# Optimization experiments

Measured on AMD Instinct MI355X. Metric: run time of the kernel, lower is better.

The kernel has to match this reference:

```python
import jax, jax.numpy as jnp
import numpy as np

N_NODES = 100000
N_EDGES = 1600000
NFEAT, NHID, NCLASS = 128, 64, 16


def setup_inputs() -> dict:
    key = jax.random.key(0)
    ks = jax.random.split(key, 6)
    x = jax.random.normal(ks[0], (N_NODES, NFEAT), dtype=jnp.float32)
    src = jax.random.randint(ks[1], (N_EDGES,), 0, N_NODES)
    dst = jax.random.randint(ks[2], (N_EDGES,), 0, N_NODES)
    # Glorot-ish init for the two GraphConv weights, zero bias (DGL default)
    W1 = jax.random.normal(ks[3], (NFEAT, NHID), dtype=jnp.float32) * (1.0 / np.sqrt(NFEAT))
    b1 = jnp.zeros((NHID,), dtype=jnp.float32)
    W2 = jax.random.normal(ks[4], (NHID, NCLASS), dtype=jnp.float32) * (1.0 / np.sqrt(NHID))
    b2 = jnp.zeros((NCLASS,), dtype=jnp.float32)
    return {"x": x, "src": src, "dst": dst, "W1": W1, "b1": b1, "W2": W2, "b2": b2}


def _graph_conv(h, W, b, src, dst, norm_src, norm_dst, n_nodes):
    """DGL GraphConv with norm='both': D_out^{-1/2} A D_in^{-1/2} h W + b.
    Apply W before aggregation when it reduces dimensionality (DGL's in>out path);
    the math is identical either way."""
    if W.shape[0] > W.shape[1]:
        h = h @ W
    h = h * norm_src[:, None]                                   # scale source feats
    agg = jax.ops.segment_sum(h[src], dst, num_segments=n_nodes)  # sparse A @ h
    agg = agg * norm_dst[:, None]
    if W.shape[0] <= W.shape[1]:
        agg = agg @ W
    return agg + b


def reference(x, src, dst, W1, b1, W2, b2):
    n = x.shape[0]
    ones = jnp.ones(src.shape, dtype=x.dtype)
    out_deg = jax.ops.segment_sum(ones, src, num_segments=n)
    in_deg = jax.ops.segment_sum(ones, dst, num_segments=n)
    norm_src = jnp.maximum(out_deg, 1.0) ** -0.5  # degree clamp as in DGL
    norm_dst = jnp.maximum(in_deg, 1.0) ** -0.5
    h = jax.nn.relu(_graph_conv(x, W1, b1, src, dst, norm_src, norm_dst, n))
    # dropout: p=0 / eval mode -> identity
    h = _graph_conv(h, W2, b2, src, dst, norm_src, norm_dst, n)
    return jax.nn.log_softmax(h, axis=1)
```

## Files before the change

### kernel.cpp

```cpp
#include <hip/hip_runtime.h>
#include <hip/hip_bf16.h>

#define NN 100000
#define NE 1600000
#define NF 128
#define NH 64
#define NC 16
#define NB1 391
#define GBIN 1280
#define CHUNK 1250
#define BBUK 196
#define NCB2 980
#define NGRP 1563

typedef __attribute__((ext_vector_type(8))) short short8v;
typedef __attribute__((ext_vector_type(4))) float float4v;

__device__ __forceinline__ float us2f(unsigned short u) {
    return __uint_as_float(((unsigned int)u) << 16);
}
__device__ __forceinline__ float bflo(unsigned u) {
    return __uint_as_float(u << 16);
}
__device__ __forceinline__ float bfhi(unsigned u) {
    return __uint_as_float(u & 0xFFFF0000u);
}
__device__ __forceinline__ unsigned short f2us_rn(float f) {
    unsigned int u = __float_as_uint(f);
    return (unsigned short)((u + 0x7FFFu + ((u >> 16) & 1u)) >> 16);
}
__device__ __forceinline__ float ldf(const void* p, size_t i, bool f32) {
    return f32 ? ((const float*)p)[i] : us2f(((const unsigned short*)p)[i]);
}

__global__ void k_sniffprep(const unsigned short* __restrict__ xu,
                            const void* __restrict__ W1,
                            unsigned short* __restrict__ W1f,
                            int* __restrict__ mode) {
    __shared__ int cnt;
    if (threadIdx.x == 0) cnt = 0;
    __syncthreads();
    int c = 0;
    for (int i = threadIdx.x; i < 4096; i += 256) {
        unsigned int e = (xu[i] >> 7) & 0xFFu;
        if (e >= 160u) c++;
    }
    atomicAdd(&cnt, c);
    __syncthreads();
    if (threadIdx.x == 0) mode[0] = (cnt >= 16) ? 1 : 0;
    __syncthreads();
    const bool f32 = (cnt >= 16);
    for (int i = threadIdx.x; i < 1024; i += 256) {
        const int kcnt = i >> 6, lane = i & 63;
        const int kc = kcnt >> 2, nt = kcnt & 3;
        const int quad = lane >> 4, col = lane & 15;
        #pragma unroll
        for (int j = 0; j < 8; ++j) {
            const size_t idx = (size_t)(kc * 32 + quad * 8 + j) * NH + nt * 16 + col;
            W1f[(size_t)i * 8 + j] = f32 ? f2us_rn(((const float*)W1)[idx])
                                         : ((const unsigned short*)W1)[idx];
        }
    }
}

__global__ void k_deg(const int4* __restrict__ src4, const int4* __restrict__ dst4,
                      int* __restrict__ deg_out, int* __restrict__ deg_in) {
    int i = blockIdx.x * blockDim.x + threadIdx.x;
    if (i < NE / 4) {
        int4 s = src4[i], d = dst4[i];
        atomicAdd(&deg_out[s.x], 1); atomicAdd(&deg_out[s.y], 1);
        atomicAdd(&deg_out[s.z], 1); atomicAdd(&deg_out[s.w], 1);
        atomicAdd(&deg_in[d.x], 1);  atomicAdd(&deg_in[d.y], 1);
        atomicAdd(&deg_in[d.z], 1);  atomicAdd(&deg_in[d.w], 1);
    }
}

__global__ void k_scatter(const int* __restrict__ src, const int* __restrict__ dst,
                          int* __restrict__ cursor, int* __restrict__ srcs_sorted) {
    int e = blockIdx.x * blockDim.x + threadIdx.x;
    if (e < NE) {
        int p = atomicAdd(&cursor[dst[e]], 1);
        srcs_sorted[p] = src[e];
    }
}

__global__ void k_scan_a(const int* __restrict__ deg_in, int* __restrict__ bsum) {
    __shared__ int s[256];
    int i = blockIdx.x * 256 + threadIdx.x;
    s[threadIdx.x] = (i < NN) ? deg_in[i] : 0;
    __syncthreads();
    for (int off = 128; off > 0; off >>= 1) {
        if (threadIdx.x < off) s[threadIdx.x] += s[threadIdx.x + off];
        __syncthreads();
    }
    if (threadIdx.x == 0) bsum[blockIdx.x] = s[0];
}

__global__ void k_scan_b(const int* __restrict__ bsum, int* __restrict__ boff) {
    __shared__ int s[512];
    int t = threadIdx.x;
    s[t] = (t < NB1) ? bsum[t] : 0;
    __syncthreads();
    for (int off = 1; off < 512; off <<= 1) {
        int v = (t >= off) ? s[t - off] : 0;
        __syncthreads();
        s[t] += v;
        __syncthreads();
    }
    if (t < NB1) boff[t] = (t == 0) ? 0 : s[t - 1];
}

__global__ void k_scan_c(const int* __restrict__ deg_in, const int* __restrict__ deg_out,
                         const int* __restrict__ boff, int* __restrict__ row_off,
                         int* __restrict__ cursor, float* __restrict__ nsrc,
                         float* __restrict__ ndst) {
    __shared__ int s[256];
    int t = threadIdx.x;
    int i = blockIdx.x * 256 + t;
    int d = (i < NN) ? deg_in[i] : 0;
    s[t] = d;
    __syncthreads();
    for (int off = 1; off < 256; off <<= 1) {
        int v = (t >= off) ? s[t - off] : 0;
        __syncthreads();
        s[t] += v;
        __syncthreads();
    }
    int excl = s[t] - d + boff[blockIdx.x];
    if (i < NN) {
        row_off[i] = excl;
        cursor[i]  = excl;
        ndst[i] = rsqrtf(fmaxf((float)d, 1.0f));
        nsrc[i] = rsqrtf(fmaxf((float)deg_out[i], 1.0f));
        if (i == NN - 1) row_off[NN] = excl + d;
    }
}

__global__ __launch_bounds__(256) void k_hist2(const int* __restrict__ src,
                                               const int* __restrict__ dst,
                                               int* __restrict__ counts_d,
                                               int* __restrict__ counts_s) {
    __shared__ int hd[BBUK], hs[BBUK];
    for (int i = threadIdx.x; i < BBUK; i += 256) { hd[i] = 0; hs[i] = 0; }
    __syncthreads();
    const int g = blockIdx.x;
    const int e0 = g * CHUNK;
    for (int i = threadIdx.x; i < CHUNK; i += 256) {
        atomicAdd(&hd[dst[e0 + i] >> 9], 1);
        atomicAdd(&hs[src[e0 + i] >> 9], 1);
    }
    __syncthreads();
    for (int i = threadIdx.x; i < BBUK; i += 256) {
        counts_d[i * GBIN + g] = hd[i];
        counts_s[i * GBIN + g] = hs[i];
    }
}

__global__ void k_cs_a(const int* __restrict__ counts, int* __restrict__ csum) {
    __shared__ int s[256];
    int i = blockIdx.x * 256 + threadIdx.x;
    s[threadIdx.x] = counts[i];
    __syncthreads();
    for (int off = 128; off > 0; off >>= 1) {
        if (threadIdx.x < off) s[threadIdx.x] += s[threadIdx.x + off];
        __syncthreads();
    }
    if (threadIdx.x == 0) csum[blockIdx.x] = s[0];
}

__global__ void k_cs_b(const int* __restrict__ csum, int* __restrict__ coff) {
    __shared__ int s[1024];
    const int t = threadIdx.x;
    const int base = blockIdx.x * NCB2;
    s[t] = (t < NCB2) ? csum[base + t] : 0;
    __syncthreads();
    for (int off = 1; off < 1024; off <<= 1) {
        int v = (t >= off) ? s[t - off] : 0;
        __syncthreads();
        s[t] += v;
        __syncthreads();
    }
    if (t < NCB2) coff[base + t] = (t == 0) ? 0 : s[t - 1];
}

__global__ void k_cs_c(int* __restrict__ counts, const int* __restrict__ coff) {
    __shared__ int s[256];
    int t = threadIdx.x;
    int i = blockIdx.x * 256 + t;
    int v = counts[i];
    s[t] = v;
    __syncthreads();
    for (int off = 1; off < 256; off <<= 1) {
        int u = (t >= off) ? s[t - off] : 0;
        __syncthreads();
        s[t] += u;
        __syncthreads();
    }
    counts[i] = s[t] - v + coff[blockIdx.x];
}

__global__ __launch_bounds__(256) void k_binscatter2(const int* __restrict__ src,
                                                     const int* __restrict__ dst,
                                                     const int* __restrict__ counts_d,
                                                     const int* __restrict__ counts_s,
                                                     unsigned int* __restrict__ packed,
                                                     unsigned short* __restrict__ packed2) {
    __shared__ int curd[BBUK], curs[BBUK];
    const int g = blockIdx.x;
    for (int i = threadIdx.x; i < BBUK; i += 256) {
        curd[i] = counts_d[i * GBIN + g];
        curs[i] = counts_s[i * GBIN + g];
    }
    __syncthreads();
    const int e0 = g * CHUNK;
    for (int i = threadIdx.x; i < CHUNK; i += 256) {
        int s = src[e0 + i], d = dst[e0 + i];
        int pd = atomicAdd(&curd[d >> 9], 1);
        packed[pd] = ((unsigned)s << 9) | (unsigned)(d & 511);
        int ps = atomicAdd(&curs[s >> 9], 1);
        packed2[ps] = (unsigned short)(s & 511);
    }
}

__global__ __launch_bounds__(256) void k_bdeg_out_nsrc(const int* __restrict__ counts_s,
                                                       const unsigned short* __restrict__ packed2,
                                                       float* __restrict__ nsrc) {
    __shared__ int h[512];
    const int b = blockIdx.x;
    const int n0 = b << 9;
    const int nlim = (NN - n0 < 512) ? (NN - n0) : 512;
    for (int j = threadIdx.x; j < 512; j += 256) h[j] = 0;
    __syncthreads();
    const int beg = counts_s[b * GBIN];
    const int end = (b + 1 < BBUK) ? counts_s[(b + 1) * GBIN] : NE;
    for (int i = beg + threadIdx.x; i < end; i += 256)
        atomicAdd(&h[packed2[i] & 511u], 1);
    __syncthreads();
    for (int j = threadIdx.x; j < nlim; j += 256)
        nsrc[n0 + j] = rsqrtf(fmaxf((float)h[j], 1.0f));
}

__global__ __launch_bounds__(256) void k_bucket_all(const int* __restrict__ counts_d,
                                                    const unsigned int* __restrict__ packed,
                                                    int* __restrict__ row_off,
                                                    float* __restrict__ ndst,
                                                    int* __restrict__ srcs_sorted) {
    __shared__ int h[512];
    const int b = blockIdx.x;
    const int n0 = b << 9;
    const int nlim = (NN - n0 < 512) ? (NN - n0) : 512;
    const int t = threadIdx.x;
    for (int j = t; j < 512; j += 256) h[j] = 0;
    __syncthreads();
    const int beg = counts_d[b * GBIN];
    const int end = (b + 1 < BBUK) ? counts_d[(b + 1) * GBIN] : NE;
    for (int i = beg + t; i < end; i += 256)
        atomicAdd(&h[packed[i] & 511u], 1);
    __syncthreads();
    const int degA = h[t], degB = h[t + 256];
    int offset = 1;
    #pragma unroll
    for (int d = 256; d > 0; d >>= 1) {
        __syncthreads();
        if (t < d) {
            int ai = offset * (2 * t + 1) - 1;
            int bi = offset * (2 * t + 2) - 1;
            h[bi] += h[ai];
        }
        offset <<= 1;
    }
    __syncthreads();
    if (t == 0) h[511] = 0;
    #pragma unroll
    for (int d = 1; d < 512; d <<= 1) {
        offset >>= 1;
        __syncthreads();
        if (t < d) {
            int ai = offset * (2 * t + 1) - 1;
            int bi = offset * (2 * t + 2) - 1;
            int tmp = h[ai]; h[ai] = h[bi]; h[bi] += tmp;
        }
    }
    __syncthreads();
    const int r0 = beg + h[t];
    const int r1 = beg + h[t + 256];
    if (t < nlim) {
        row_off[n0 + t] = r0;
        ndst[n0 + t] = rsqrtf(fmaxf((float)degA, 1.0f));
    }
    if (t + 256 < nlim) {
        row_off[n0 + t + 256] = r1;
        ndst[n0 + t + 256] = rsqrtf(fmaxf((float)degB, 1.0f));
    }
    if (n0 + nlim == NN && t == 0) row_off[NN] = end;
    __syncthreads();
    h[t] = r0; h[t + 256] = r1;
    __syncthreads();
    for (int i = beg + t; i < end; i += 256) {
        unsigned v = packed[i];
        int p = atomicAdd(&h[v & 511u], 1);
        srcs_sorted[p] = (int)(v >> 9);
    }
}

__global__ __launch_bounds__(256) void k_gemm1_mfma(
    const void* __restrict__ x, const unsigned short* __restrict__ W1f,
    const float* __restrict__ nsrc, unsigned short* __restrict__ h1,
    const int* __restrict__ mode)
{
    const bool f32 = (mode[0] != 0);
    const int tid = threadIdx.x;
    const int wave = tid >> 6, lane = tid & 63;
    const int col = lane & 15, quad = lane >> 4;

    short8v bfrag[16];
    #pragma unroll
    for (int f = 0; f < 16; ++f)
        bfrag[f] = *(const short8v*)(W1f + ((size_t)f * 64 + lane) * 8);

    const int base = blockIdx.x * 64 + wave * 16;
    int arow = base + col;
    if (arow > NN - 1) arow = NN - 1;

    short8v afrag[4];
    if (f32) {
        const float4* ap = (const float4*)((const float*)x + (size_t)arow * NF);
        #pragma unroll
        for (int kc = 0; kc < 4; ++kc) {
            float4 v0 = ap[kc * 8 + quad * 2];
            float4 v1 = ap[kc * 8 + quad * 2 + 1];
            short8v af;
            af[0] = (short)f2us_rn(v0.x); af[1] = (short)f2us_rn(v0.y);
            af[2] = (short)f2us_rn(v0.z); af[3] = (short)f2us_rn(v0.w);
            af[4] = (short)f2us_rn(v1.x); af[5] = (short)f2us_rn(v1.y);
            af[6] = (short)f2us_rn(v1.z); af[7] = (short)f2us_rn(v1.w);
            afrag[kc] = af;
        }
    } else {
        const uint4* ap = (const uint4*)((const unsigned short*)x + (size_t)arow * NF);
        #pragma unroll
        for (int kc = 0; kc < 4; ++kc) {
            uint4 v = ap[kc * 4 + quad];
            afrag[kc] = *reinterpret_cast<const short8v*>(&v);
        }
    }

    float4v acc[4];
    #pragma unroll
    for (int nt = 0; nt < 4; ++nt) acc[nt] = (float4v){0.f, 0.f, 0.f, 0.f};
    #pragma unroll
    for (int kc = 0; kc < 4; ++kc)
        #pragma unroll
        for (int nt = 0; nt < 4; ++nt)
            acc[nt] = __builtin_amdgcn_mfma_f32_16x16x32_bf16(afrag[kc], bfrag[kc * 4 + nt], acc[nt], 0, 0, 0);

    #pragma unroll
    for (int reg = 0; reg < 4; ++reg) {
        const int row = base + quad * 4 + reg;
        if (row < NN) {
            const float ns = nsrc[row];
            unsigned short* hp = h1 + (size_t)row * NH + col;
            hp[0]  = f2us_rn(acc[0][reg] * ns);
            hp[16] = f2us_rn(acc[1][reg] * ns);
            hp[32] = f2us_rn(acc[2][reg] * ns);
            hp[48] = f2us_rn(acc[3][reg] * ns);
        }
    }
}

__global__ __launch_bounds__(256) void k_agg1csr(
    const int* __restrict__ row_off, const int* __restrict__ srcs,
    const unsigned short* __restrict__ h1, const float* __restrict__ ndst,
    const float* __restrict__ nsrc, const void* __restrict__ b1,
    const void* __restrict__ W2, const int* __restrict__ mode,
    unsigned short* __restrict__ h2)
{
    const bool f32 = (mode[0] != 0);
    const int lane = threadIdx.x & 63;
    const int q  = lane >> 4;
    const int li = lane & 15;

    const float bias0 = ldf(b1, 4*li+0, f32), bias1 = ldf(b1, 4*li+1, f32);
    const float bias2 = ldf(b1, 4*li+2, f32), bias3 = ldf(b1, 4*li+3, f32);
    float w2[4][4];
    #pragma unroll
    for (int j = 0; j < 4; ++j)
        #pragma unroll
        for (int m = 0; m < 4; ++m)
            w2[j][m] = ldf(W2, (size_t)(4*li+j)*NC + (q + 4*m), f32);

    const int wid = (blockIdx.x * blockDim.x + threadIdx.x) >> 6;
    const int nw  = (gridDim.x * blockDim.x) >> 6;
    const uint2* __restrict__ h1v = (const uint2*)h1;
    const unsigned uli = (unsigned)li;

    int row = wid;
    if (row >= NN) return;
    int beg = row_off[row];
    int end = row_off[row + 1];
    float nd = ndst[row];
    float ns = nsrc[row];

    while (row < NN) {
        const int nrow = row + nw;
        int nbeg = 0, nend = 0;
        float nnd = 0.f, nns = 0.f;
        if (nrow < NN) {
            nbeg = row_off[nrow];
            nend = row_off[nrow + 1];
            nnd  = ndst[nrow];
            nns  = nsrc[nrow];
        }

        float ax = 0.f, ay = 0.f, az = 0.f, aw = 0.f;
        float bx = 0.f, by = 0.f, bz = 0.f, bw = 0.f;
        const int e1 = end - 1;
        int i = beg + q;
        while (i < end) {
            const int j1 = i + 4, j2 = i + 8, j3 = i + 12;
            const int t1 = (j1 < end) ? j1 : e1;
            const int t2 = (j2 < end) ? j2 : e1;
            const int t3 = (j3 < end) ? j3 : e1;
            const int s0 = srcs[(unsigned)i];
            const int s1 = srcs[(unsigned)t1];
            const int s2 = srcs[(unsigned)t2];
            const int s3 = srcs[(unsigned)t3];
            const uint2 v0 = h1v[(unsigned)s0 * 16u + uli];
            const uint2 v1 = h1v[(unsigned)s1 * 16u + uli];
            const uint2 v2 = h1v[(unsigned)s2 * 16u + uli];
            const uint2 v3 = h1v[(unsigned)s3 * 16u + uli];
            ax += bflo(v0.x); ay += bfhi(v0.x);
            az += bflo(v0.y); aw += bfhi(v0.y);
            if (j1 < end) {
                bx += bflo(v1.x); by += bfhi(v1.x);
                bz += bflo(v1.y); bw += bfhi(v1.y);
            }
            if (j2 < end) {
                ax += bflo(v2.x); ay += bfhi(v2.x);
                az += bflo(v2.y); aw += bfhi(v2.y);
            }
            if (j3 < end) {
                bx += bflo(v3.x); by += bfhi(v3.x);
                bz += bflo(v3.y); bw += bfhi(v3.y);
            }
            i += 16;
        }
        ax += bx; ay += by; az += bz; aw += bw;
        ax += __shfl_xor(ax, 16); ay += __shfl_xor(ay, 16);
        az += __shfl_xor(az, 16); aw += __shfl_xor(aw, 16);
        ax += __shfl_xor(ax, 32); ay += __shfl_xor(ay, 32);
        az += __shfl_xor(az, 32); aw += __shfl_xor(aw, 32);

        const float t0 = fmaxf(fmaf(ax, nd, bias0), 0.f);
        const float t1f = fmaxf(fmaf(ay, nd, bias1), 0.f);
        const float t2f = fmaxf(fmaf(az, nd, bias2), 0.f);
        const float t3f = fmaxf(fmaf(aw, nd, bias3), 0.f);

        float p0 = fmaf(t0,w2[0][0],fmaf(t1f,w2[1][0],fmaf(t2f,w2[2][0],t3f*w2[3][0])));
        float p1 = fmaf(t0,w2[0][1],fmaf(t1f,w2[1][1],fmaf(t2f,w2[2][1],t3f*w2[3][1])));
        float p2 = fmaf(t0,w2[0][2],fmaf(t1f,w2[1][2],fmaf(t2f,w2[2][2],t3f*w2[3][2])));
        float p3 = fmaf(t0,w2[0][3],fmaf(t1f,w2[1][3],fmaf(t2f,w2[2][3],t3f*w2[3][3])));
        #pragma unroll
        for (int off = 1; off <= 8; off <<= 1) {
            p0 += __shfl_xor(p0, off);
            p1 += __shfl_xor(p1, off);
            p2 += __shfl_xor(p2, off);
            p3 += __shfl_xor(p3, off);
        }
        if (li < 4) {
            float v = (li == 0) ? p0 : (li == 1) ? p1 : (li == 2) ? p2 : p3;
            h2[(size_t)row * NC + q + 4*li] = f2us_rn(v * ns);
        }

        row = nrow; beg = nbeg; end = nend; nd = nnd; ns = nns;
    }
}

__global__ __launch_bounds__(256) void k_out(
    const int* __restrict__ row_off, const int* __restrict__ srcs,
    const unsigned short* __restrict__ h2, const float* __restrict__ ndst,
    const void* __restrict__ b2, const int* __restrict__ mode,
    void* __restrict__ out)
{
    const bool f32 = (mode[0] != 0);
    const int lane = threadIdx.x & 63;
    const int q  = lane >> 3;
    const int li = lane & 7;
    const float b2v0 = ldf(b2, 2*li,   f32);
    const float b2v1 = ldf(b2, 2*li+1, f32);

    const int wid = (blockIdx.x * blockDim.x + threadIdx.x) >> 6;
    const int nw  = (gridDim.x * blockDim.x) >> 6;
    const unsigned* __restrict__ h2v = (const unsigned*)h2;
    const unsigned uli = (unsigned)li;

    int row = wid;
    if (row >= NN) return;
    int beg = row_off[row];
    int end = row_off[row + 1];
    float nd = ndst[row];

    while (row < NN) {
        const int nrow = row + nw;
        int nbeg = 0, nend = 0;
        float nnd = 0.f;
        if (nrow < NN) {
            nbeg = row_off[nrow];
            nend = row_off[nrow + 1];
            nnd  = ndst[nrow];
        }

        float a0 = 0.f, a1 = 0.f, c0 = 0.f, c1 = 0.f;
        const int e1 = end - 1;
        int i = beg + q;
        while (i < end) {
            const int j1 = i + 8;
            const int t1 = (j1 < end) ? j1 : e1;
            const int s0 = srcs[(unsigned)i];
            const int s1 = srcs[(unsigned)t1];
            const unsigned u0 = h2v[(unsigned)s0 * 8u + uli];
            const unsigned u1 = h2v[(unsigned)s1 * 8u + uli];
            a0 += bflo(u0); a1 += bfhi(u0);
            if (j1 < end) {
                c0 += bflo(u1); c1 += bfhi(u1);
            }
            i += 16;
        }
        a0 += c0; a1 += c1;
        #pragma unroll
        for (int off = 8; off <= 32; off <<= 1) {
            a0 += __shfl_xor(a0, off);
            a1 += __shfl_xor(a1, off);
        }
        float v0 = fmaf(a0, nd, b2v0);
        float v1 = fmaf(a1, nd, b2v1);
        float m = fmaxf(v0, v1);
        #pragma unroll
        for (int off = 1; off <= 4; off <<= 1) m = fmaxf(m, __shfl_xor(m, off));
        float sm = __expf(v0 - m) + __expf(v1 - m);
        #pragma unroll
        for (int off = 1; off <= 4; off <<= 1) sm += __shfl_xor(sm, off);
        const float lsm = __logf(sm);
        const float r0 = v0 - m - lsm, r1 = v1 - m - lsm;
        if (q == 0) {
            if (f32) {
                float2 o; o.x = r0; o.y = r1;
                *(float2*)((float*)out + (size_t)row * NC + 2*li) = o;
            } else {
                unsigned o = ((unsigned)f2us_rn(r1) << 16) | (unsigned)f2us_rn(r0);
                *(unsigned*)((unsigned short*)out + (size_t)row * NC + 2*li) = o;
            }
        }

        row = nrow; beg = nbeg; end = nend; nd = nnd;
    }
}

extern "C" void kernel_launch(void* const* d_in, const int* in_sizes, int n_in,
                              void* d_out, int out_size, void* d_ws, size_t ws_size,
                              hipStream_t stream) {
    const void* x  = d_in[0];
    const int* src = (const int*)d_in[1];
    const int* dst = (const int*)d_in[2];
    const void* W1 = d_in[3];
    const void* b1 = d_in[4];
    const void* W2 = d_in[5];
    const void* b2 = d_in[6];

    char* ws = (char*)d_ws;
    const size_t O_MODE = 0;
    const size_t O_W1F  = 1024;
    const size_t O_CNT  = O_W1F + 16384;
    const size_t O_CS   = O_CNT  + 401408;
    const size_t O_DEG  = O_CS   + 4096;
    const size_t O_NSRC = O_DEG  + 800000;
    const size_t O_NDST = O_NSRC + 400000;
    const size_t O_ROW  = O_NDST + 400000;
    const size_t O_CUR  = O_ROW  + 400128;
    const size_t O_BS   = O_CUR  + 400128;
    const size_t O_SRCS = O_BS   + 4096;
    const size_t O_H2   = O_SRCS + 6400000;
    const size_t O_H1   = O_H2   + 3200000;
    const size_t O_CNT2 = O_H1 + 9600000;
    const size_t NEED = O_H1 + 12800000;
    const bool fast_csr = ws_size >= NEED;

    int*   mode     = (int*)(ws + O_MODE);
    unsigned short* W1f = (unsigned short*)(ws + O_W1F);
    int*   counts_d = (int*)(ws + O_CNT2);
    int*   counts_s = counts_d + BBUK * GBIN;
    int*   csum     = (int*)(ws + O_CS);
    int*   coff     = (int*)(ws + O_CS + 8192);
    int*   deg_out  = (int*)(ws + O_DEG);
    int*   deg_in   = deg_out + NN;
    float* nsrc     = (float*)(ws + O_NSRC);
    float* ndst     = (float*)(ws + O_NDST);
    int*   row_off  = (int*)(ws + O_ROW);
    int*   cursor   = (int*)(ws + O_CUR);
    int*   bsum     = (int*)(ws + O_BS);
    int*   boff     = (int*)(ws + O_BS + 2048);
    int*   srcs_s   = (int*)(ws + O_SRCS);
    unsigned short* h2 = (unsigned short*)(ws + O_H2);
    unsigned short* h1 = (unsigned short*)(ws + O_H1);
    unsigned int*   packed  = (unsigned int*)(ws + O_H1);
    unsigned short* packed2 = (unsigned short*)(ws + O_H1 + 6400000);

    k_sniffprep<<<1, 256, 0, stream>>>((const unsigned short*)x, W1, W1f, mode);
    if (fast_csr) {
        k_hist2<<<GBIN, 256, 0, stream>>>(src, dst, counts_d, counts_s);
        k_cs_a<<<2 * NCB2, 256, 0, stream>>>(counts_d, csum);
        k_cs_b<<<2, 1024, 0, stream>>>(csum, coff);
        k_cs_c<<<2 * NCB2, 256, 0, stream>>>(counts_d, coff);
        k_binscatter2<<<GBIN, 256, 0, stream>>>(src, dst, counts_d, counts_s, packed, packed2);
        k_bdeg_out_nsrc<<<BBUK, 256, 0, stream>>>(counts_s, packed2, nsrc);
        k_bucket_all<<<BBUK, 256, 0, stream>>>(counts_d, packed, row_off, ndst, srcs_s);
    } else {
        hipMemsetAsync(deg_out, 0, 2 * (size_t)NN * sizeof(int), stream);
        k_deg<<<(NE / 4 + 255) / 256, 256, 0, stream>>>((const int4*)src, (const int4*)dst, deg_out, deg_in);
        k_scan_a<<<NB1, 256, 0, stream>>>(deg_in, bsum);
        k_scan_b<<<1, 512, 0, stream>>>(bsum, boff);
        k_scan_c<<<NB1, 256, 0, stream>>>(deg_in, deg_out, boff, row_off, cursor, nsrc, ndst);
        k_scatter<<<(NE + 255) / 256, 256, 0, stream>>>(src, dst, cursor, srcs_s);
    }
    k_gemm1_mfma<<<NGRP, 256, 0, stream>>>(x, W1f, nsrc, h1, mode);
    k_agg1csr<<<2048, 256, 0, stream>>>(row_off, srcs_s, h1, ndst, nsrc, b1, W2, mode, h2);
    k_out<<<2048, 256, 0, stream>>>(row_off, srcs_s, h2, ndst, b2, mode, d_out);
}
```

Baseline: 290.3 us.

## Compute out-degrees with global atomics and drop the source-side bucket sort

Out-degree is no longer derived from a second bucketed scatter of source indices (packed2 plus a per-bucket histogram kernel). Instead k_hist2 does global atomicAdds into a deg_out array, and k_bucket_all computes nsrc from it. deg_out is zeroed in an enlarged sniffprep launch. The edge chunking also changes to 256 larger chunks, which shrinks the count-scan kernels. This removes one scatter pass and one kernel but adds contended global atomics and gives fewer blocks for the histogram and scatter passes.

```diff
diff --git a/kernel.cpp b/kernel.cpp
--- a/kernel.cpp
+++ b/kernel.cpp
@@ -7,10 +7,10 @@
 #define NH 64
 #define NC 16
 #define NB1 391
-#define GBIN 1280
-#define CHUNK 1250
+#define GBIN 256
+#define CHUNK 6250
 #define BBUK 196
-#define NCB2 980
+#define NCB 196
 #define NGRP 1563
 
 typedef __attribute__((ext_vector_type(8))) short short8v;
@@ -36,7 +36,11 @@
 __global__ void k_sniffprep(const unsigned short* __restrict__ xu,
                             const void* __restrict__ W1,
                             unsigned short* __restrict__ W1f,
-                            int* __restrict__ mode) {
+                            int* __restrict__ mode,
+                            int* __restrict__ deg_out) {
+    for (int i = blockIdx.x * 256 + threadIdx.x; i < NN; i += gridDim.x * 256)
+        deg_out[i] = 0;
+    if (blockIdx.x != 0) return;
     __shared__ int cnt;
     if (threadIdx.x == 0) cnt = 0;
     __syncthreads();
@@ -139,21 +143,19 @@
 __global__ __launch_bounds__(256) void k_hist2(const int* __restrict__ src,
                                                const int* __restrict__ dst,
                                                int* __restrict__ counts_d,
-                                               int* __restrict__ counts_s) {
-    __shared__ int hd[BBUK], hs[BBUK];
-    for (int i = threadIdx.x; i < BBUK; i += 256) { hd[i] = 0; hs[i] = 0; }
+                                               int* __restrict__ deg_out) {
+    __shared__ int hd[BBUK];
+    for (int i = threadIdx.x; i < BBUK; i += 256) hd[i] = 0;
     __syncthreads();
     const int g = blockIdx.x;
     const int e0 = g * CHUNK;
     for (int i = threadIdx.x; i < CHUNK; i += 256) {
         atomicAdd(&hd[dst[e0 + i] >> 9], 1);
-        atomicAdd(&hs[src[e0 + i] >> 9], 1);
-    }
-    __syncthreads();
-    for (int i = threadIdx.x; i < BBUK; i += 256) {
+        atomicAdd(&deg_out[src[e0 + i]], 1);
+    }
+    __syncthreads();
+    for (int i = threadIdx.x; i < BBUK; i += 256)
         counts_d[i * GBIN + g] = hd[i];
-        counts_s[i * GBIN + g] = hs[i];
-    }
 }
 
 __global__ void k_cs_a(const int* __restrict__ counts, int* __restrict__ csum) {
@@ -169,18 +171,17 @@
 }
 
 __global__ void k_cs_b(const int* __restrict__ csum, int* __restrict__ coff) {
-    __shared__ int s[1024];
+    __shared__ int s[256];
     const int t = threadIdx.x;
-    const int base = blockIdx.x * NCB2;
-    s[t] = (t < NCB2) ? csum[base + t] : 0;
-    __syncthreads();
-    for (int off = 1; off < 1024; off <<= 1) {
+    s[t] = (t < NCB) ? csum[t] : 0;
+    __syncthreads();
+    for (int off = 1; off < 256; off <<= 1) {
         int v = (t >= off) ? s[t - off] : 0;
         __syncthreads();
         s[t] += v;
         __syncthreads();
     }
-    if (t < NCB2) coff[base + t] = (t == 0) ? 0 : s[t - 1];
+    if (t < NCB) coff[t] = (t == 0) ? 0 : s[t - 1];
 }
 
 __global__ void k_cs_c(int* __restrict__ counts, const int* __restrict__ coff) {
@@ -199,51 +200,29 @@
     counts[i] = s[t] - v + coff[blockIdx.x];
 }
 
-__global__ __launch_bounds__(256) void k_binscatter2(const int* __restrict__ src,
-                                                     const int* __restrict__ dst,
-                                                     const int* __restrict__ counts_d,
-                                                     const int* __restrict__ counts_s,
-                                                     unsigned int* __restrict__ packed,
-                                                     unsigned short* __restrict__ packed2) {
-    __shared__ int curd[BBUK], curs[BBUK];
+__global__ __launch_bounds__(256) void k_binscatter(const int* __restrict__ src,
+                                                    const int* __restrict__ dst,
+                                                    const int* __restrict__ counts_d,
+                                                    unsigned int* __restrict__ packed) {
+    __shared__ int curd[BBUK];
     const int g = blockIdx.x;
-    for (int i = threadIdx.x; i < BBUK; i += 256) {
+    for (int i = threadIdx.x; i < BBUK; i += 256)
         curd[i] = counts_d[i * GBIN + g];
-        curs[i] = counts_s[i * GBIN + g];
-    }
     __syncthreads();
     const int e0 = g * CHUNK;
     for (int i = threadIdx.x; i < CHUNK; i += 256) {
         int s = src[e0 + i], d = dst[e0 + i];
         int pd = atomicAdd(&curd[d >> 9], 1);
         packed[pd] = ((unsigned)s << 9) | (unsigned)(d & 511);
-        int ps = atomicAdd(&curs[s >> 9], 1);
-        packed2[ps] = (unsigned short)(s & 511);
-    }
-}
-
-__global__ __launch_bounds__(256) void k_bdeg_out_nsrc(const int* __restrict__ counts_s,
-                                                       const unsigned short* __restrict__ packed2,
-                                                       float* __restrict__ nsrc) {
-    __shared__ int h[512];
-    const int b = blockIdx.x;
-    const int n0 = b << 9;
-    const int nlim = (NN - n0 < 512) ? (NN - n0) : 512;
-    for (int j = threadIdx.x; j < 512; j += 256) h[j] = 0;
-    __syncthreads();
-    const int beg = counts_s[b * GBIN];
-    const int end = (b + 1 < BBUK) ? counts_s[(b + 1) * GBIN] : NE;
-    for (int i = beg + threadIdx.x; i < end; i += 256)
-        atomicAdd(&h[packed2[i] & 511u], 1);
-    __syncthreads();
-    for (int j = threadIdx.x; j < nlim; j += 256)
-        nsrc[n0 + j] = rsqrtf(fmaxf((float)h[j], 1.0f));
+    }
 }
 
 __global__ __launch_bounds__(256) void k_bucket_all(const int* __restrict__ counts_d,
                                                     const unsigned int* __restrict__ packed,
+                                                    const int* __restrict__ deg_out,
                                                     int* __restrict__ row_off,
                                                     float* __restrict__ ndst,
+                                                    float* __restrict__ nsrc,
                                                     int* __restrict__ srcs_sorted) {
     __shared__ int h[512];
     const int b = blockIdx.x;
@@ -287,10 +266,12 @@
     if (t < nlim) {
         row_off[n0 + t] = r0;
         ndst[n0 + t] = rsqrtf(fmaxf((float)degA, 1.0f));
+        nsrc[n0 + t] = rsqrtf(fmaxf((float)deg_out[n0 + t], 1.0f));
     }
     if (t + 256 < nlim) {
         row_off[n0 + t + 256] = r1;
         ndst[n0 + t + 256] = rsqrtf(fmaxf((float)degB, 1.0f));
+        nsrc[n0 + t + 256] = rsqrtf(fmaxf((float)deg_out[n0 + t + 256], 1.0f));
     }
     if (n0 + nlim == NN && t == 0) row_off[NN] = end;
     __syncthreads();
@@ -581,16 +562,14 @@
     const size_t O_SRCS = O_BS   + 4096;
     const size_t O_H2   = O_SRCS + 6400000;
     const size_t O_H1   = O_H2   + 3200000;
-    const size_t O_CNT2 = O_H1 + 9600000;
     const size_t NEED = O_H1 + 12800000;
     const bool fast_csr = ws_size >= NEED;
 
     int*   mode     = (int*)(ws + O_MODE);
     unsigned short* W1f = (unsigned short*)(ws + O_W1F);
-    int*   counts_d = (int*)(ws + O_CNT2);
-    int*   counts_s = counts_d + BBUK * GBIN;
+    int*   counts_d = (int*)(ws + O_CNT);
     int*   csum     = (int*)(ws + O_CS);
-    int*   coff     = (int*)(ws + O_CS + 8192);
+    int*   coff     = (int*)(ws + O_CS + 2048);
     int*   deg_out  = (int*)(ws + O_DEG);
     int*   deg_in   = deg_out + NN;
     float* nsrc     = (float*)(ws + O_NSRC);
@@ -603,17 +582,15 @@
     unsigned short* h2 = (unsigned short*)(ws + O_H2);
     unsigned short* h1 = (unsigned short*)(ws + O_H1);
     unsigned int*   packed  = (unsigned int*)(ws + O_H1);
-    unsigned short* packed2 = (unsigned short*)(ws + O_H1 + 6400000);
-
-    k_sniffprep<<<1, 256, 0, stream>>>((const unsigned short*)x, W1, W1f, mode);
+
+    k_sniffprep<<<64, 256, 0, stream>>>((const unsigned short*)x, W1, W1f, mode, deg_out);
     if (fast_csr) {
-        k_hist2<<<GBIN, 256, 0, stream>>>(src, dst, counts_d, counts_s);
-        k_cs_a<<<2 * NCB2, 256, 0, stream>>>(counts_d, csum);
-        k_cs_b<<<2, 1024, 0, stream>>>(csum, coff);
-        k_cs_c<<<2 * NCB2, 256, 0, stream>>>(counts_d, coff);
-        k_binscatter2<<<GBIN, 256, 0, stream>>>(src, dst, counts_d, counts_s, packed, packed2);
-        k_bdeg_out_nsrc<<<BBUK, 256, 0, stream>>>(counts_s, packed2, nsrc);
-        k_bucket_all<<<BBUK, 256, 0, stream>>>(counts_d, packed, row_off, ndst, srcs_s);
+        k_hist2<<<GBIN, 256, 0, stream>>>(src, dst, counts_d, deg_out);
+        k_cs_a<<<NCB, 256, 0, stream>>>(counts_d, csum);
+        k_cs_b<<<1, 256, 0, stream>>>(csum, coff);
+        k_cs_c<<<NCB, 256, 0, stream>>>(counts_d, coff);
+        k_binscatter<<<GBIN, 256, 0, stream>>>(src, dst, counts_d, packed);
+        k_bucket_all<<<BBUK, 256, 0, stream>>>(counts_d, packed, deg_out, row_off, ndst, nsrc, srcs_s);
     } else {
         hipMemsetAsync(deg_out, 0, 2 * (size_t)NN * sizeof(int), stream);
         k_deg<<<(NE / 4 + 255) / 256, 256, 0, stream>>>((const int4*)src, (const int4*)dst, deg_out, deg_in);
```

Result: slower. 315.1 us (+8.5%).
